# Kernel optimization log

Hardware: AMD Instinct MI355X
Metric: run time of the kernel (lower is better)

Reference implementation:

```python
import jax, jax.numpy as jnp
import numpy as np

B, C, K, F = 16, 64, 128, 6
HORIZON_S = 3.0  # conflict_horizon_s default
EPS = 1e-06


def setup_inputs() -> dict:
    rng = np.random.default_rng(0)
    # base adjacency: sparse random directed graph, zero diagonal
    A = (rng.random((B, K, K)) < 0.05).astype(np.float32)
    A[:, np.arange(K), np.arange(K)] = 0.0
    # candidates: exactly one unordered-pair edit (state in {0:none,1:i->j,2:j->i})
    cand = np.repeat(A[:, None], C, axis=1).copy()
    i = rng.integers(0, K - 1, (B, C))
    j = i + 1 + (rng.integers(0, K - 1, (B, C)) % (K - 1 - i))
    state = rng.integers(0, 3, (B, C))
    bidx = np.arange(B)[:, None] * np.ones((1, C), dtype=np.int64)
    cidx = np.ones((B, 1), dtype=np.int64) * np.arange(C)[None, :]
    cand[bidx, cidx, i, j] = (state == 1).astype(np.float32)
    cand[bidx, cidx, j, i] = (state == 2).astype(np.float32)
    cand[:, 0] = A  # candidate 0 is NOOP (keep A_t)
    # agent features: (x, y, yaw, vx, vy, pad)
    feat = rng.normal(size=(B, K, F)).astype(np.float32)
    feat[..., 0:2] *= 20.0  # spread positions over ~40m
    mask = (rng.random((B, K)) > 0.1).astype(np.float32)
    return {
        "A_t": jnp.asarray(A),
        "candidate_A": jnp.asarray(cand),
        "agent_feat": jnp.asarray(feat),
        "agent_mask": jnp.asarray(mask),
    }


def _edit_tokens(A_t, candidate_A):
    # vectorized version of EBSTM.extract_edit_tokens
    Bn, Cn, Kn, _ = candidate_A.shape
    base = A_t > 0.5                      # [B,K,K]
    cb = candidate_A > 0.5                # [B,C,K,K]
    diff = cb != base[:, None]            # [B,C,K,K]
    upper = jnp.triu(jnp.ones((Kn, Kn), dtype=bool), k=1)
    pairdiff = (diff | jnp.swapaxes(diff, -1, -2)) & upper
    flat = pairdiff.reshape(Bn, Cn, Kn * Kn)
    changed = flat.any(-1)                # [B,C]
    idx = jnp.argmax(flat, axis=-1)       # first changed pair in row-major (i,j) order
    i = idx // Kn
    j = idx % Kn
    barange = jnp.arange(Bn)[:, None]
    carange = jnp.arange(Cn)[None, :]
    b_ij = base[barange, i, j]
    b_ji = base[barange, j, i]
    c_ij = cb[barange, carange, i, j]
    c_ji = cb[barange, carange, j, i]
    prev = jnp.where(b_ij & ~b_ji, 1, jnp.where(b_ji & ~b_ij, 2, 0))
    nxt = jnp.where(c_ij & ~c_ji, 1, jnp.where(c_ji & ~c_ij, 2, 0))
    tokens = jnp.stack([i, j, prev, nxt], axis=-1).astype(jnp.int32)
    return tokens * changed[..., None].astype(jnp.int32)


def _relation_state3(cb):
    # cb: bool [B,C,K,K]
    at = jnp.swapaxes(cb, -1, -2)
    return ((cb & ~at).astype(jnp.int32) * 1
            + (~cb & at).astype(jnp.int32) * 2
            + (cb & at).astype(jnp.int32) * 3)


def _batched_acyclic(cb, agent_mask):
    # vectorized Kahn zero-indegree peel, matching EBSTM._is_acyclic semantics:
    #  - indegree counts edges from ALL sources (valid or not)
    #  - only valid nodes are ever removed
    #  - special case: <=1 valid node is acyclic
    Bn, Cn, Kn, _ = cb.shape
    valid = (agent_mask > 0.5)[:, None, :]           # [B,1,K]
    Ai = cb.astype(jnp.int32)                        # [B,C,K,K]
    indeg = Ai.sum(axis=-2) * valid.astype(jnp.int32)  # [B,C,K]
    removed = jnp.zeros((Bn, Cn, Kn), dtype=bool)

    def body(t, carry):
        indeg, removed = carry
        rem = valid & (~removed) & (indeg == 0)
        dec = jnp.einsum('bci,bcij->bcj', rem.astype(jnp.int32), Ai)
        return indeg - dec, removed | rem

    indeg, removed = jax.lax.fori_loop(0, Kn, body, (indeg, removed))
    vcount = valid.astype(jnp.int32).sum(-1)          # [B,1]
    return (removed.astype(jnp.int32).sum(-1) == vcount) | (vcount <= 1)


def _pair_dists(agent_feat):
    pos = agent_feat[..., 0:2]
    vel = agent_feat[..., 3:5]
    # _pair_distance: d[b,i,j] = |pos_i - pos_j|
    d = jnp.linalg.norm(pos[:, :, None] - pos[:, None, :], axis=-1)
    # _pair_closest_approach_distance: r[b,i,j] = pos_j - pos_i
    r = pos[:, None, :] - pos[:, :, None]
    v = vel[:, None, :] - vel[:, :, None]
    vv = (v * v).sum(-1)
    rv = (r * v).sum(-1)
    t_star = jnp.clip(-rv / (vv + EPS), 0.0, HORIZON_S)
    dmin = jnp.linalg.norm(r + v * t_star[..., None], axis=-1)
    eye = jnp.eye(dmin.shape[-1], dtype=bool)[None]
    dmin = jnp.where(eye, jnp.inf, dmin)
    return jnp.stack([d, dmin], axis=0)  # [2,B,K,K]


def reference(A_t, candidate_A, agent_feat, agent_mask):
    cb = candidate_A > 0.5
    tokens = _edit_tokens(A_t, candidate_A)          # [B,C,4] int32
    rel = _relation_state3(cb)                       # [B,C,K,K] int32
    acyclic = _batched_acyclic(cb, agent_mask)       # [B,C] bool
    dists = _pair_dists(agent_feat)                  # [2,B,K,K] float32
    return tokens, rel, acyclic, dists
```

## Files before the change

### kernel.cpp

```cpp
#include <hip/hip_runtime.h>
#include <cstdint>
#include <math.h>

#define KN 128
#define BATCH 16
#define CAND 64

typedef float vfloat4 __attribute__((ext_vector_type(4)));

static constexpr size_t TOK_OFF = 0;
static constexpr size_t REL_OFF = (size_t)BATCH * CAND * 4;
static constexpr size_t ACY_OFF = REL_OFF + (size_t)BATCH * CAND * KN * KN;
static constexpr size_t DST_OFF = ACY_OFF + (size_t)BATCH * CAND;

#define DIAG_BIG 1.0e30f

__global__ __launch_bounds__(256) void prep_kernel(const float* __restrict__ A_t,
                                                   const float* __restrict__ feat,
                                                   uint32_t* __restrict__ bits,
                                                   float* __restrict__ out) {
    int t = threadIdx.x;
    {
        int tid  = blockIdx.x * 256 + t;
        int wave = tid >> 6;
        int lane = tid & 63;
        int half = wave & 1;
        int row  = wave >> 1;
        float v = A_t[(size_t)row * KN + half * 64 + lane];
        unsigned long long m = __ballot(v > 0.5f);
        if (lane == 0) {
            bits[row * 4 + half * 2]     = (uint32_t)m;
            bits[row * 4 + half * 2 + 1] = (uint32_t)(m >> 32);
        }
    }
    {
        int bi = 2 * blockIdx.x + (t >> 7);
        int b2 = bi >> 7, i = bi & 127, j = t & 127;
        const float* fi = feat + (size_t)bi * 6;
        const float* fj = feat + (size_t)(b2 * KN + j) * 6;
        float pix = fi[0], piy = fi[1], vix = fi[3], viy = fi[4];
        float pjx = fj[0], pjy = fj[1], vjx = fj[3], vjy = fj[4];
        float dx = pix - pjx, dy = piy - pjy;
        float d = sqrtf(dx * dx + dy * dy);
        float rx = pjx - pix, ry = pjy - piy;
        float vx = vjx - vix, vy = vjy - viy;
        float vv = vx * vx + vy * vy;
        float rv = rx * vx + ry * vy;
        float ts = fminf(fmaxf(-rv / (vv + 1e-6f), 0.0f), 3.0f);
        float mx = rx + vx * ts, my = ry + vy * ts;
        float dmin = (i == j) ? DIAG_BIG : sqrtf(mx * mx + my * my);
        float* o = out + DST_OFF;
        __builtin_nontemporal_store(d,    o + (size_t)(b2 * KN + i) * KN + j);
        __builtin_nontemporal_store(dmin, o + (size_t)((BATCH + b2) * KN + i) * KN + j);
    }
}

__global__ __launch_bounds__(256) void main_kernel(const float* __restrict__ cand,
                                                   const float* __restrict__ mask,
                                                   const uint32_t* __restrict__ baseBits,
                                                   float* __restrict__ out) {
    __shared__ uint32_t adj[KN][5];
    __shared__ uint32_t adjT[KN][6];
    __shared__ uint32_t baseB[KN][4];
    __shared__ uint32_t validW[4];
    __shared__ uint32_t remW[4];
    __shared__ uint32_t removedW[4];
    __shared__ int      minIdx;

    const int t    = threadIdx.x;
    const int lane = t & 63;
    const int wave = t >> 6;
    const int bc   = blockIdx.x;
    const int b    = bc >> 6;

    const float* cptr = cand + (size_t)bc * (KN * KN);
    float* relp = out + REL_OFF + (size_t)bc * (KN * KN);

    float4 c[16];
    const int sub = lane & 31;
    #pragma unroll
    for (int m = 0; m < 16; ++m) {
        int r = (m * 4 + wave) * 2 + (lane >> 5);
        c[m] = ((const float4*)(cptr + (size_t)r * KN))[sub];
    }

    if (t == 0) minIdx = 0x7fffffff;
    if (t < 4)  removedW[t] = 0;

    for (int w = t; w < 512; w += 256) {
        baseB[w >> 2][w & 3] = baseBits[b * 512 + w];
    }

    if (wave < 2) {
        float mv = mask[b * KN + wave * 64 + lane];
        unsigned long long m = __ballot(mv > 0.5f);
        if (lane == 0) {
            validW[wave * 2]     = (uint32_t)m;
            validW[wave * 2 + 1] = (uint32_t)(m >> 32);
        }
    }

    #pragma unroll
    for (int m = 0; m < 16; ++m) {
        int r = (m * 4 + wave) * 2 + (lane >> 5);
        const float4 v = c[m];
        uint32_t nib = (v.x > 0.5f ? 1u : 0u) | (v.y > 0.5f ? 2u : 0u) |
                       (v.z > 0.5f ? 4u : 0u) | (v.w > 0.5f ? 8u : 0u);
        uint32_t word = nib << (4 * (sub & 7));
        word |= __shfl_xor(word, 1);
        word |= __shfl_xor(word, 2);
        word |= __shfl_xor(word, 4);
        if ((lane & 7) == 0) adj[r][sub >> 3] = word;
    }
    __syncthreads();

    {
        const int h = wave >> 1, q = wave & 1;
        uint32_t rw0 = adj[h * 64 + lane][q * 2];
        uint32_t rw1 = adj[h * 64 + lane][q * 2 + 1];
        uint32_t myLo = 0, myHi = 0;
        #pragma unroll
        for (int cc = 0; cc < 64; ++cc) {
            uint32_t w = (cc < 32) ? rw0 : rw1;
            unsigned long long m = __ballot((w >> (cc & 31)) & 1u);
            if (lane == cc) { myLo = (uint32_t)m; myHi = (uint32_t)(m >> 32); }
        }
        adjT[q * 64 + lane][2 * h]     = myLo;
        adjT[q * 64 + lane][2 * h + 1] = myHi;
    }
    __syncthreads();

    uint32_t cT0 = 0, cT1 = 0, cT2 = 0, cT3 = 0;
    int  indeg = 0;
    bool validT = false;
    if (t < KN) {
        cT0 = adjT[t][0]; cT1 = adjT[t][1]; cT2 = adjT[t][2]; cT3 = adjT[t][3];
        validT = (validW[t >> 5] >> (t & 31)) & 1u;
        indeg = validT ? (__popc(cT0) + __popc(cT1) + __popc(cT2) + __popc(cT3)) : 0;
    }

    auto rel_expand = [&]() {
        #pragma unroll
        for (int m = 0; m < 16; ++m) {
            int q  = t + 256 * m;
            int i  = q >> 5;
            int j0 = (q & 31) * 4;
            int iw = j0 >> 5, sh = j0 & 31;
            uint32_t wij = adj[i][iw];
            uint32_t wti = adjT[i][iw];
            uint32_t a4 = (wij >> sh) & 0xFu;
            uint32_t b4 = (wti >> sh) & 0xFu;
            uint32_t packed = ((a4 * 0x00204081u) & 0x01010101u)
                            | (((b4 * 0x00204081u) & 0x01010101u) << 1);
            vfloat4 o;
            o.x = (float)(uint8_t)(packed);
            o.y = (float)(uint8_t)(packed >> 8);
            o.z = (float)(uint8_t)(packed >> 16);
            o.w = (float)(uint8_t)(packed >> 24);
            __builtin_nontemporal_store(o, ((vfloat4*)relp) + q);
        }
    };

    auto logic_phase = [&]() {
        for (int idx = t; idx < 512; idx += 256) {
            int i = idx >> 2, k = idx & 3;
            uint32_t diff = adj[i][k] ^ baseB[i][k];
            if (diff) {
                int base = k * 32;
                uint32_t up, low;
                if (i < base)            { up = diff; low = 0u; }
                else if (i >= base + 31) { up = 0u; low = (i > base + 31) ? diff : (diff & 0x7fffffffu); }
                else {
                    int s = i - base;
                    up  = diff & (0xffffffffu << (s + 1));
                    low = diff & ((1u << s) - 1u);
                }
                int c1 = 0x7fffffff, c2 = 0x7fffffff;
                if (up)  c1 = (i << 7) | (base + __builtin_ctz(up));
                if (low) { int cc2 = base + __builtin_ctz(low); c2 = (cc2 << 7) | i; }
                int cm = min(c1, c2);
                if (cm != 0x7fffffff) atomicMin(&minIdx, cm);
            }
        }
        __syncthreads();

        if (t == 0) {
            float* tok = out + TOK_OFF + (size_t)bc * 4;
            int mi = minIdx;
            if (mi != 0x7fffffff) {
                int i = mi >> 7, j = mi & 127;
                uint32_t b_ij = (baseB[i][j >> 5] >> (j & 31)) & 1u;
                uint32_t b_ji = (baseB[j][i >> 5] >> (i & 31)) & 1u;
                uint32_t c_ij = (adj[i][j >> 5] >> (j & 31)) & 1u;
                uint32_t c_ji = (adj[j][i >> 5] >> (i & 31)) & 1u;
                int prev = (b_ij && !b_ji) ? 1 : ((b_ji && !b_ij) ? 2 : 0);
                int nxt  = (c_ij && !c_ji) ? 1 : ((c_ji && !c_ij) ? 2 : 0);
                tok[0] = (float)i; tok[1] = (float)j; tok[2] = (float)prev; tok[3] = (float)nxt;
            } else {
                tok[0] = 0.f; tok[1] = 0.f; tok[2] = 0.f; tok[3] = 0.f;
            }
        }

        bool removed = false;
        for (int it = 0; it < KN; ++it) {
            bool rem = (t < KN) && validT && !removed && (indeg == 0);
            unsigned long long m = __ballot(rem);
            if (wave < 2 && lane == 0) {
                remW[wave * 2]     = (uint32_t)m;
                remW[wave * 2 + 1] = (uint32_t)(m >> 32);
            }
            __syncthreads();
            uint32_t r0 = remW[0], r1 = remW[1], r2 = remW[2], r3 = remW[3];
            if ((r0 | r1 | r2 | r3) == 0u) break;
            if (t < 4) removedW[t] |= remW[t];
            if (t < KN) {
                indeg -= __popc(r0 & cT0) + __popc(r1 & cT1) +
                         __popc(r2 & cT2) + __popc(r3 & cT3);
                removed = removed || rem;
            }
            __syncthreads();
        }
        __syncthreads();

        if (t == 0) {
            int rc = __popc(removedW[0]) + __popc(removedW[1]) + __popc(removedW[2]) + __popc(removedW[3]);
            int vc = __popc(validW[0]) + __popc(validW[1]) + __popc(validW[2]) + __popc(validW[3]);
            out[ACY_OFF + bc] = ((rc == vc) || (vc <= 1)) ? 1.0f : 0.0f;
        }
    };

    if ((bc & 1) == 0) {
        rel_expand();
        logic_phase();
    } else {
        logic_phase();
        rel_expand();
    }
}

extern "C" void kernel_launch(void* const* d_in, const int* in_sizes, int n_in,
                              void* d_out, int out_size, void* d_ws, size_t ws_size,
                              hipStream_t stream) {
    const float* A_t  = (const float*)d_in[0];
    const float* cand = (const float*)d_in[1];
    const float* feat = (const float*)d_in[2];
    const float* mask = (const float*)d_in[3];
    float* out = (float*)d_out;
    uint32_t* bits = (uint32_t*)d_ws;

    prep_kernel<<<1024, 256, 0, stream>>>(A_t, feat, bits, out);
    main_kernel<<<BATCH * CAND, 256, 0, stream>>>(cand, mask, bits, out);
}
```

Before: 120.5 us.

## Process two candidates per block and prefetch second candidate during first's work

Each block now handles a pair of candidates. The second candidate's loads are issued right after the first is packed, so global reads overlap with the transpose, relation expansion and acyclicity loop of the first. Full __syncthreads are replaced with a custom barrier that waits only on LDS counters, which lets outstanding global loads and stores run across barriers. The grid is halved and launch bounds request two blocks per CU, so the extra registers for the prefetch may reduce occupancy and there are fewer blocks to fill the GPU.

```diff
diff --git a/kernel.cpp b/kernel.cpp
--- a/kernel.cpp
+++ b/kernel.cpp
@@ -14,6 +14,13 @@
 static constexpr size_t DST_OFF = ACY_OFF + (size_t)BATCH * CAND;
 
 #define DIAG_BIG 1.0e30f
+
+#define LBAR() do {                                         \
+    __builtin_amdgcn_sched_barrier(0);                      \
+    asm volatile("s_waitcnt lgkmcnt(0)" ::: "memory");      \
+    __builtin_amdgcn_s_barrier();                           \
+    __builtin_amdgcn_sched_barrier(0);                      \
+} while (0)
 
 __global__ __launch_bounds__(256) void prep_kernel(const float* __restrict__ A_t,
                                                    const float* __restrict__ feat,
@@ -55,42 +62,38 @@
     }
 }
 
-__global__ __launch_bounds__(256) void main_kernel(const float* __restrict__ cand,
-                                                   const float* __restrict__ mask,
-                                                   const uint32_t* __restrict__ baseBits,
-                                                   float* __restrict__ out) {
+__global__ __launch_bounds__(256, 2) void main_kernel(const float* __restrict__ cand,
+                                                      const float* __restrict__ mask,
+                                                      const uint32_t* __restrict__ baseBits,
+                                                      float* __restrict__ out) {
     __shared__ uint32_t adj[KN][5];
     __shared__ uint32_t adjT[KN][6];
     __shared__ uint32_t baseB[KN][4];
     __shared__ uint32_t validW[4];
     __shared__ uint32_t remW[4];
-    __shared__ uint32_t removedW[4];
-    __shared__ int      minIdx;
+    __shared__ uint32_t removedW2[2][4];
+    __shared__ int      minIdx2[2];
 
     const int t    = threadIdx.x;
     const int lane = t & 63;
     const int wave = t >> 6;
-    const int bc   = blockIdx.x;
-    const int b    = bc >> 6;
-
-    const float* cptr = cand + (size_t)bc * (KN * KN);
-    float* relp = out + REL_OFF + (size_t)bc * (KN * KN);
-
-    float4 c[16];
-    const int sub = lane & 31;
-    #pragma unroll
-    for (int m = 0; m < 16; ++m) {
-        int r = (m * 4 + wave) * 2 + (lane >> 5);
-        c[m] = ((const float4*)(cptr + (size_t)r * KN))[sub];
-    }
-
-    if (t == 0) minIdx = 0x7fffffff;
-    if (t < 4)  removedW[t] = 0;
-
-    for (int w = t; w < 512; w += 256) {
-        baseB[w >> 2][w & 3] = baseBits[b * 512 + w];
-    }
-
+    const int pair = blockIdx.x;
+    const int bc0  = pair * 2;
+    const int b    = bc0 >> 6;
+
+    const float* cptr0 = cand + (size_t)bc0 * (KN * KN);
+    const float* cptr1 = cptr0 + (KN * KN);
+    float* relp0 = out + REL_OFF + (size_t)bc0 * (KN * KN);
+    float* relp1 = relp0 + (KN * KN);
+
+    if (t == 0) { minIdx2[0] = 0x7fffffff; minIdx2[1] = 0x7fffffff; }
+    if (t < 8)  ((uint32_t*)removedW2)[t] = 0;
+    {
+        uint32_t w0 = baseBits[b * 512 + t];
+        uint32_t w1 = baseBits[b * 512 + 256 + t];
+        ((uint32_t*)baseB)[t]       = w0;
+        ((uint32_t*)baseB)[t + 256] = w1;
+    }
     if (wave < 2) {
         float mv = mask[b * KN + wave * 64 + lane];
         unsigned long long m = __ballot(mv > 0.5f);
@@ -100,21 +103,31 @@
         }
     }
 
+    const int sub = lane & 31;
+
+    float4 c0[16];
     #pragma unroll
     for (int m = 0; m < 16; ++m) {
         int r = (m * 4 + wave) * 2 + (lane >> 5);
-        const float4 v = c[m];
-        uint32_t nib = (v.x > 0.5f ? 1u : 0u) | (v.y > 0.5f ? 2u : 0u) |
-                       (v.z > 0.5f ? 4u : 0u) | (v.w > 0.5f ? 8u : 0u);
-        uint32_t word = nib << (4 * (sub & 7));
-        word |= __shfl_xor(word, 1);
-        word |= __shfl_xor(word, 2);
-        word |= __shfl_xor(word, 4);
-        if ((lane & 7) == 0) adj[r][sub >> 3] = word;
-    }
-    __syncthreads();
-
-    {
+        c0[m] = ((const float4*)(cptr0 + (size_t)r * KN))[sub];
+    }
+
+    auto pack = [&](const float4* cc) {
+        #pragma unroll
+        for (int m = 0; m < 16; ++m) {
+            int r = (m * 4 + wave) * 2 + (lane >> 5);
+            const float4 v = cc[m];
+            uint32_t nib = (v.x > 0.5f ? 1u : 0u) | (v.y > 0.5f ? 2u : 0u) |
+                           (v.z > 0.5f ? 4u : 0u) | (v.w > 0.5f ? 8u : 0u);
+            uint32_t word = nib << (4 * (sub & 7));
+            word |= __shfl_xor(word, 1);
+            word |= __shfl_xor(word, 2);
+            word |= __shfl_xor(word, 4);
+            if ((lane & 7) == 0) adj[r][sub >> 3] = word;
+        }
+    };
+
+    auto transpose = [&]() {
         const int h = wave >> 1, q = wave & 1;
         uint32_t rw0 = adj[h * 64 + lane][q * 2];
         uint32_t rw1 = adj[h * 64 + lane][q * 2 + 1];
@@ -127,19 +140,9 @@
         }
         adjT[q * 64 + lane][2 * h]     = myLo;
         adjT[q * 64 + lane][2 * h + 1] = myHi;
-    }
-    __syncthreads();
-
-    uint32_t cT0 = 0, cT1 = 0, cT2 = 0, cT3 = 0;
-    int  indeg = 0;
-    bool validT = false;
-    if (t < KN) {
-        cT0 = adjT[t][0]; cT1 = adjT[t][1]; cT2 = adjT[t][2]; cT3 = adjT[t][3];
-        validT = (validW[t >> 5] >> (t & 31)) & 1u;
-        indeg = validT ? (__popc(cT0) + __popc(cT1) + __popc(cT2) + __popc(cT3)) : 0;
-    }
-
-    auto rel_expand = [&]() {
+    };
+
+    auto rel_expand = [&](float* relp) {
         #pragma unroll
         for (int m = 0; m < 16; ++m) {
             int q  = t + 256 * m;
@@ -161,8 +164,10 @@
         }
     };
 
-    auto logic_phase = [&]() {
-        for (int idx = t; idx < 512; idx += 256) {
+    auto logic = [&](int bcX, int km) {
+        #pragma unroll
+        for (int rep = 0; rep < 2; ++rep) {
+            int idx = t + rep * 256;
             int i = idx >> 2, k = idx & 3;
             uint32_t diff = adj[i][k] ^ baseB[i][k];
             if (diff) {
@@ -179,14 +184,14 @@
                 if (up)  c1 = (i << 7) | (base + __builtin_ctz(up));
                 if (low) { int cc2 = base + __builtin_ctz(low); c2 = (cc2 << 7) | i; }
                 int cm = min(c1, c2);
-                if (cm != 0x7fffffff) atomicMin(&minIdx, cm);
-            }
-        }
-        __syncthreads();
+                if (cm != 0x7fffffff) atomicMin(&minIdx2[km], cm);
+            }
+        }
+        LBAR();
 
         if (t == 0) {
-            float* tok = out + TOK_OFF + (size_t)bc * 4;
-            int mi = minIdx;
+            float* tok = out + TOK_OFF + (size_t)bcX * 4;
+            int mi = minIdx2[km];
             if (mi != 0x7fffffff) {
                 int i = mi >> 7, j = mi & 127;
                 uint32_t b_ij = (baseB[i][j >> 5] >> (j & 31)) & 1u;
@@ -201,6 +206,15 @@
             }
         }
 
+        uint32_t cT0 = 0, cT1 = 0, cT2 = 0, cT3 = 0;
+        int  indeg = 0;
+        bool validT = false;
+        if (t < KN) {
+            cT0 = adjT[t][0]; cT1 = adjT[t][1]; cT2 = adjT[t][2]; cT3 = adjT[t][3];
+            validT = (validW[t >> 5] >> (t & 31)) & 1u;
+            indeg = validT ? (__popc(cT0) + __popc(cT1) + __popc(cT2) + __popc(cT3)) : 0;
+        }
+
         bool removed = false;
         for (int it = 0; it < KN; ++it) {
             bool rem = (t < KN) && validT && !removed && (indeg == 0);
@@ -209,33 +223,53 @@
                 remW[wave * 2]     = (uint32_t)m;
                 remW[wave * 2 + 1] = (uint32_t)(m >> 32);
             }
-            __syncthreads();
+            LBAR();
             uint32_t r0 = remW[0], r1 = remW[1], r2 = remW[2], r3 = remW[3];
             if ((r0 | r1 | r2 | r3) == 0u) break;
-            if (t < 4) removedW[t] |= remW[t];
+            if (t < 4) removedW2[km][t] |= remW[t];
             if (t < KN) {
                 indeg -= __popc(r0 & cT0) + __popc(r1 & cT1) +
                          __popc(r2 & cT2) + __popc(r3 & cT3);
                 removed = removed || rem;
             }
-            __syncthreads();
-        }
-        __syncthreads();
+            LBAR();
+        }
+        LBAR();
 
         if (t == 0) {
-            int rc = __popc(removedW[0]) + __popc(removedW[1]) + __popc(removedW[2]) + __popc(removedW[3]);
-            int vc = __popc(validW[0]) + __popc(validW[1]) + __popc(validW[2]) + __popc(validW[3]);
-            out[ACY_OFF + bc] = ((rc == vc) || (vc <= 1)) ? 1.0f : 0.0f;
-        }
-    };
-
-    if ((bc & 1) == 0) {
-        rel_expand();
-        logic_phase();
-    } else {
-        logic_phase();
-        rel_expand();
-    }
+            int rc = __popc(removedW2[km][0]) + __popc(removedW2[km][1]) +
+                     __popc(removedW2[km][2]) + __popc(removedW2[km][3]);
+            int vc = __popc(validW[0]) + __popc(validW[1]) +
+                     __popc(validW[2]) + __popc(validW[3]);
+            out[ACY_OFF + bcX] = ((rc == vc) || (vc <= 1)) ? 1.0f : 0.0f;
+        }
+    };
+
+    pack(c0);
+
+    float4 c1[16];
+    #pragma unroll
+    for (int m = 0; m < 16; ++m) {
+        int r = (m * 4 + wave) * 2 + (lane >> 5);
+        c1[m] = ((const float4*)(cptr1 + (size_t)r * KN))[sub];
+    }
+
+    LBAR();
+    transpose();
+    LBAR();
+
+    const int par = (pair >> 8) & 1;
+    if (par == 0) { rel_expand(relp0); logic(bc0, 0); }
+    else          { logic(bc0, 0);     rel_expand(relp0); }
+
+    LBAR();
+    pack(c1);
+    LBAR();
+    transpose();
+    LBAR();
+
+    if (par == 0) { logic(bc0 + 1, 1); rel_expand(relp1); }
+    else          { rel_expand(relp1); logic(bc0 + 1, 1); }
 }
 
 extern "C" void kernel_launch(void* const* d_in, const int* in_sizes, int n_in,
@@ -249,5 +283,5 @@
     uint32_t* bits = (uint32_t*)d_ws;
 
     prep_kernel<<<1024, 256, 0, stream>>>(A_t, feat, bits, out);
-    main_kernel<<<BATCH * CAND, 256, 0, stream>>>(cand, mask, bits, out);
+    main_kernel<<<(BATCH * CAND) / 2, 256, 0, stream>>>(cand, mask, bits, out);
 }
```

Result: slower. 126.2 us (+4.8%).

## Use butterfly shuffle transpose, double-buffer Kahn loop flags, change phase ordering

Applied to the files above, without the earlier changes.

Replaces the 64-step ballot transpose of the adjacency bit matrix with a 6-stage butterfly shuffle transpose on 64-bit words. The peeling loop's removal mask is double-buffered so one of the two barriers per iteration can be dropped. The rule choosing whether a block runs the rel expansion or the logic phase first now uses bit 8 of the block index instead of parity, which changes how memory-heavy and logic-heavy blocks interleave. The double-buffering has to stay race-free across iterations, and the new phase-order split may balance load differently.

```diff
diff --git a/kernel.cpp b/kernel.cpp
--- a/kernel.cpp
+++ b/kernel.cpp
@@ -63,7 +63,7 @@
     __shared__ uint32_t adjT[KN][6];
     __shared__ uint32_t baseB[KN][4];
     __shared__ uint32_t validW[4];
-    __shared__ uint32_t remW[4];
+    __shared__ uint32_t remW2[2][4];
     __shared__ uint32_t removedW[4];
     __shared__ int      minIdx;
 
@@ -116,17 +116,22 @@
 
     {
         const int h = wave >> 1, q = wave & 1;
-        uint32_t rw0 = adj[h * 64 + lane][q * 2];
-        uint32_t rw1 = adj[h * 64 + lane][q * 2 + 1];
-        uint32_t myLo = 0, myHi = 0;
+        uint32_t lo = adj[h * 64 + lane][q * 2];
+        uint32_t hi = adj[h * 64 + lane][q * 2 + 1];
+        unsigned long long x = ((unsigned long long)hi << 32) | lo;
+        const unsigned long long Lm[6] = {
+            0x5555555555555555ull, 0x3333333333333333ull, 0x0F0F0F0F0F0F0F0Full,
+            0x00FF00FF00FF00FFull, 0x0000FFFF0000FFFFull, 0x00000000FFFFFFFFull };
         #pragma unroll
-        for (int cc = 0; cc < 64; ++cc) {
-            uint32_t w = (cc < 32) ? rw0 : rw1;
-            unsigned long long m = __ballot((w >> (cc & 31)) & 1u);
-            if (lane == cc) { myLo = (uint32_t)m; myHi = (uint32_t)(m >> 32); }
-        }
-        adjT[q * 64 + lane][2 * h]     = myLo;
-        adjT[q * 64 + lane][2 * h + 1] = myHi;
+        for (int k = 0; k < 6; ++k) {
+            const int d = 1 << k;
+            const unsigned long long L = Lm[k];
+            unsigned long long y = __shfl_xor((unsigned long long)x, d);
+            x = (lane & d) ? ((x & ~L) | ((y & ~L) >> d))
+                           : ((x & L)  | ((y & L) << d));
+        }
+        adjT[q * 64 + lane][2 * h]     = (uint32_t)x;
+        adjT[q * 64 + lane][2 * h + 1] = (uint32_t)(x >> 32);
     }
     __syncthreads();
 
@@ -203,22 +208,23 @@
 
         bool removed = false;
         for (int it = 0; it < KN; ++it) {
+            const int bsel = it & 1;
             bool rem = (t < KN) && validT && !removed && (indeg == 0);
             unsigned long long m = __ballot(rem);
             if (wave < 2 && lane == 0) {
-                remW[wave * 2]     = (uint32_t)m;
-                remW[wave * 2 + 1] = (uint32_t)(m >> 32);
+                remW2[bsel][wave * 2]     = (uint32_t)m;
+                remW2[bsel][wave * 2 + 1] = (uint32_t)(m >> 32);
             }
             __syncthreads();
-            uint32_t r0 = remW[0], r1 = remW[1], r2 = remW[2], r3 = remW[3];
+            uint32_t r0 = remW2[bsel][0], r1 = remW2[bsel][1];
+            uint32_t r2 = remW2[bsel][2], r3 = remW2[bsel][3];
             if ((r0 | r1 | r2 | r3) == 0u) break;
-            if (t < 4) removedW[t] |= remW[t];
+            if (t < 4) removedW[t] |= remW2[bsel][t];
             if (t < KN) {
                 indeg -= __popc(r0 & cT0) + __popc(r1 & cT1) +
                          __popc(r2 & cT2) + __popc(r3 & cT3);
                 removed = removed || rem;
             }
-            __syncthreads();
         }
         __syncthreads();
 
@@ -229,7 +235,7 @@
         }
     };
 
-    if ((bc & 1) == 0) {
+    if (((bc >> 8) & 1) == 0) {
         rel_expand();
         logic_phase();
     } else {
```

Result: slower. 123.4 us (+2.4%).

## Fuse prep and main kernels into a single launch

Applied to the files above, without the earlier changes.

Merges the separate prep kernel, which bit-packs the base adjacency and computes the pair distances, into the main per-candidate kernel. Each block now bit-packs its own copy of the batch's base adjacency from A_t directly into shared memory and computes one slice of the distance output. This removes a kernel launch, the inter-kernel dependency and the workspace round trip. In exchange, every candidate block reads the full 64KB base matrix, which is redundant but likely served from cache, and carries extra registers for a second 16-entry float4 array, which may lower occupancy.

```diff
diff --git a/kernel.cpp b/kernel.cpp
--- a/kernel.cpp
+++ b/kernel.cpp
@@ -15,31 +15,57 @@
 
 #define DIAG_BIG 1.0e30f
 
-__global__ __launch_bounds__(256) void prep_kernel(const float* __restrict__ A_t,
-                                                   const float* __restrict__ feat,
-                                                   uint32_t* __restrict__ bits,
-                                                   float* __restrict__ out) {
-    int t = threadIdx.x;
+__global__ __launch_bounds__(256) void fused_kernel(const float* __restrict__ A_t,
+                                                    const float* __restrict__ cand,
+                                                    const float* __restrict__ feat,
+                                                    const float* __restrict__ mask,
+                                                    float* __restrict__ out) {
+    __shared__ uint32_t adj[KN][5];
+    __shared__ uint32_t adjT[KN][6];
+    __shared__ uint32_t baseB[KN][4];
+    __shared__ uint32_t validW[4];
+    __shared__ uint32_t remW[4];
+    __shared__ uint32_t removedW[4];
+    __shared__ int      minIdx;
+
+    const int t    = threadIdx.x;
+    const int lane = t & 63;
+    const int wave = t >> 6;
+    const int bc   = blockIdx.x;
+    const int b    = bc >> 6;
+
+    const float* cptr = cand + (size_t)bc * (KN * KN);
+    const float* aptr = A_t  + (size_t)b  * (KN * KN);
+    float* relp = out + REL_OFF + (size_t)bc * (KN * KN);
+
+    const int bi = 2 * bc + (t >> 7);
+    const int b2 = bi >> 7, di = bi & 127, dj = t & 127;
+    const float* fi = feat + (size_t)bi * 6;
+    const float* fj = feat + (size_t)(b2 * KN + dj) * 6;
+    float pix = fi[0], piy = fi[1], vix = fi[3], viy = fi[4];
+    float pjx = fj[0], pjy = fj[1], vjx = fj[3], vjy = fj[4];
+
+    float4 c[16];
+    const int sub = lane & 31;
+    #pragma unroll
+    for (int m = 0; m < 16; ++m) {
+        int r = (m * 4 + wave) * 2 + (lane >> 5);
+        c[m] = ((const float4*)(cptr + (size_t)r * KN))[sub];
+    }
+
+    if (t == 0) minIdx = 0x7fffffff;
+    if (t < 4)  removedW[t] = 0;
+
+    if (wave < 2) {
+        float mv = mask[b * KN + wave * 64 + lane];
+        unsigned long long m = __ballot(mv > 0.5f);
+        if (lane == 0) {
+            validW[wave * 2]     = (uint32_t)m;
+            validW[wave * 2 + 1] = (uint32_t)(m >> 32);
+        }
+    }
+
     {
-        int tid  = blockIdx.x * 256 + t;
-        int wave = tid >> 6;
-        int lane = tid & 63;
-        int half = wave & 1;
-        int row  = wave >> 1;
-        float v = A_t[(size_t)row * KN + half * 64 + lane];
-        unsigned long long m = __ballot(v > 0.5f);
-        if (lane == 0) {
-            bits[row * 4 + half * 2]     = (uint32_t)m;
-            bits[row * 4 + half * 2 + 1] = (uint32_t)(m >> 32);
-        }
-    }
-    {
-        int bi = 2 * blockIdx.x + (t >> 7);
-        int b2 = bi >> 7, i = bi & 127, j = t & 127;
-        const float* fi = feat + (size_t)bi * 6;
-        const float* fj = feat + (size_t)(b2 * KN + j) * 6;
-        float pix = fi[0], piy = fi[1], vix = fi[3], viy = fi[4];
-        float pjx = fj[0], pjy = fj[1], vjx = fj[3], vjy = fj[4];
         float dx = pix - pjx, dy = piy - pjy;
         float d = sqrtf(dx * dx + dy * dy);
         float rx = pjx - pix, ry = pjy - piy;
@@ -48,56 +74,10 @@
         float rv = rx * vx + ry * vy;
         float ts = fminf(fmaxf(-rv / (vv + 1e-6f), 0.0f), 3.0f);
         float mx = rx + vx * ts, my = ry + vy * ts;
-        float dmin = (i == j) ? DIAG_BIG : sqrtf(mx * mx + my * my);
+        float dmin = (di == dj) ? DIAG_BIG : sqrtf(mx * mx + my * my);
         float* o = out + DST_OFF;
-        __builtin_nontemporal_store(d,    o + (size_t)(b2 * KN + i) * KN + j);
-        __builtin_nontemporal_store(dmin, o + (size_t)((BATCH + b2) * KN + i) * KN + j);
-    }
-}
-
-__global__ __launch_bounds__(256) void main_kernel(const float* __restrict__ cand,
-                                                   const float* __restrict__ mask,
-                                                   const uint32_t* __restrict__ baseBits,
-                                                   float* __restrict__ out) {
-    __shared__ uint32_t adj[KN][5];
-    __shared__ uint32_t adjT[KN][6];
-    __shared__ uint32_t baseB[KN][4];
-    __shared__ uint32_t validW[4];
-    __shared__ uint32_t remW[4];
-    __shared__ uint32_t removedW[4];
-    __shared__ int      minIdx;
-
-    const int t    = threadIdx.x;
-    const int lane = t & 63;
-    const int wave = t >> 6;
-    const int bc   = blockIdx.x;
-    const int b    = bc >> 6;
-
-    const float* cptr = cand + (size_t)bc * (KN * KN);
-    float* relp = out + REL_OFF + (size_t)bc * (KN * KN);
-
-    float4 c[16];
-    const int sub = lane & 31;
-    #pragma unroll
-    for (int m = 0; m < 16; ++m) {
-        int r = (m * 4 + wave) * 2 + (lane >> 5);
-        c[m] = ((const float4*)(cptr + (size_t)r * KN))[sub];
-    }
-
-    if (t == 0) minIdx = 0x7fffffff;
-    if (t < 4)  removedW[t] = 0;
-
-    for (int w = t; w < 512; w += 256) {
-        baseB[w >> 2][w & 3] = baseBits[b * 512 + w];
-    }
-
-    if (wave < 2) {
-        float mv = mask[b * KN + wave * 64 + lane];
-        unsigned long long m = __ballot(mv > 0.5f);
-        if (lane == 0) {
-            validW[wave * 2]     = (uint32_t)m;
-            validW[wave * 2 + 1] = (uint32_t)(m >> 32);
-        }
+        __builtin_nontemporal_store(d,    o + (size_t)(b2 * KN + di) * KN + dj);
+        __builtin_nontemporal_store(dmin, o + (size_t)((BATCH + b2) * KN + di) * KN + dj);
     }
 
     #pragma unroll
@@ -112,6 +92,14 @@
         word |= __shfl_xor(word, 4);
         if ((lane & 7) == 0) adj[r][sub >> 3] = word;
     }
+
+    float4 a[16];
+    #pragma unroll
+    for (int m = 0; m < 16; ++m) {
+        int r = (m * 4 + wave) * 2 + (lane >> 5);
+        a[m] = ((const float4*)(aptr + (size_t)r * KN))[sub];
+    }
+
     __syncthreads();
 
     {
@@ -128,6 +116,20 @@
         adjT[q * 64 + lane][2 * h]     = myLo;
         adjT[q * 64 + lane][2 * h + 1] = myHi;
     }
+
+    #pragma unroll
+    for (int m = 0; m < 16; ++m) {
+        int r = (m * 4 + wave) * 2 + (lane >> 5);
+        const float4 v = a[m];
+        uint32_t nib = (v.x > 0.5f ? 1u : 0u) | (v.y > 0.5f ? 2u : 0u) |
+                       (v.z > 0.5f ? 4u : 0u) | (v.w > 0.5f ? 8u : 0u);
+        uint32_t word = nib << (4 * (sub & 7));
+        word |= __shfl_xor(word, 1);
+        word |= __shfl_xor(word, 2);
+        word |= __shfl_xor(word, 4);
+        if ((lane & 7) == 0) baseB[r][sub >> 3] = word;
+    }
+
     __syncthreads();
 
     uint32_t cT0 = 0, cT1 = 0, cT2 = 0, cT3 = 0;
@@ -246,8 +248,7 @@
     const float* feat = (const float*)d_in[2];
     const float* mask = (const float*)d_in[3];
     float* out = (float*)d_out;
-    uint32_t* bits = (uint32_t*)d_ws;
-
-    prep_kernel<<<1024, 256, 0, stream>>>(A_t, feat, bits, out);
-    main_kernel<<<BATCH * CAND, 256, 0, stream>>>(cand, mask, bits, out);
+    (void)d_ws; (void)ws_size;
+
+    fused_kernel<<<BATCH * CAND, 256, 0, stream>>>(A_t, cand, feat, mask, out);
 }
```

After: 123.2 us. 2.3% more time.
